# Performance work log

Hardware: AMD Instinct MI355X
Metric: run time of the kernel (lower is better)

Reference implementation:

```python
import jax, jax.numpy as jnp
import numpy as np

N = 50000          # nodes
E = 800000         # edges (avg degree 16)
DIN = 128          # d_input
H = 8              # heads per layer
D = 16             # per-head hidden dim
HID = H * D        # 128
ALPHA = 0.2        # LeakyReLU negative slope in GAT attention
BN_EPS = 1e-5


def _xavier(key, shape):
    fan_in, fan_out = shape[0], shape[-1]
    lim = np.sqrt(6.0 / (fan_in + fan_out)).astype(np.float32)
    return jax.random.uniform(key, shape, jnp.float32, -lim, lim)


def setup_inputs() -> dict:
    key = jax.random.key(0)
    ks = jax.random.split(key, 8)
    x = jax.random.normal(ks[0], (N, DIN), jnp.float32)
    edge_idx = jax.random.randint(ks[1], (2, E), 0, N)
    W1 = _xavier(ks[2], (DIN, HID))
    a1 = _xavier(ks[3], (H, 2 * D))
    W2 = _xavier(ks[4], (HID, HID))
    a2 = _xavier(ks[5], (H, 2 * D))
    W3 = _xavier(ks[6], (HID, HID))
    a3 = _xavier(ks[7], (H, 2 * D))
    ones = jnp.ones((HID,), jnp.float32)
    zeros = jnp.zeros((HID,), jnp.float32)
    return {"x": x, "edge_idx": edge_idx,
            "W1": W1, "a1": a1, "W2": W2, "a2": a2, "W3": W3, "a3": a3,
            "g1": ones, "b1": zeros, "g2": ones, "b2": zeros, "g3": ones, "b3": zeros}


def _leaky(x):
    return jnp.where(x >= 0, x, ALPHA * x)


def _gat_layer(x, src, dst, W, a):
    # x: [N, Fin]; W: [Fin, H*D]; a: [H, 2D]
    h = (x @ W).reshape(-1, H, D)                       # [N, H, D]
    e_src = jnp.einsum('nhd,hd->nh', h, a[:, :D])       # a^T part for source node
    e_dst = jnp.einsum('nhd,hd->nh', h, a[:, D:])       # a^T part for destination node
    e = _leaky(e_src[src] + e_dst[dst])                 # [E, H]
    m = jax.ops.segment_max(e, dst, num_segments=N)     # per-dst stable softmax max
    m = jnp.where(jnp.isfinite(m), m, 0.0)              # empty segments -> 0
    w = jnp.exp(e - m[dst])                             # [E, H]
    den = jax.ops.segment_sum(w, dst, num_segments=N)   # [N, H]
    agg = jax.ops.segment_sum(h[src] * w[:, :, None], dst, num_segments=N)  # [N, H, D]
    out = agg / (den[:, :, None] + 1e-16)
    return out.reshape(-1, HID)                         # concat heads


def _bn(x, g, b):
    # BatchNorm1d training-mode math over the node axis
    mu = x.mean(axis=0)
    var = x.var(axis=0)
    return g * (x - mu) * jax.lax.rsqrt(var + BN_EPS) + b


def reference(x, edge_idx, W1, a1, W2, a2, W3, a3, g1, b1, g2, b2, g3, b3):
    src, dst = edge_idx[0], edge_idx[1]
    h1 = jax.nn.elu(_bn(_gat_layer(x, src, dst, W1, a1), g1, b1))
    h2 = jax.nn.elu(_bn(_gat_layer(h1, src, dst, W2, a2), g2, b2))
    h3_in = h1 + h2  # skip connection
    return _bn(_gat_layer(h3_in, src, dst, W3, a3), g3, b3)
```

## Files before the change

### kernel.cpp

```cpp
#include <hip/hip_runtime.h>
#include <hip/hip_bf16.h>
#include <hip/hip_fp16.h>
#include <cstddef>

#define NNODES 50000
#define NEDGES 800000
#define HID 128
#define NHEAD 8
#define AGG_NB (NNODES / 4)
#define NSLICE 64
#define SLAYER (NSLICE * 512)

#define NBUCK 196
#define BCH 2048
#define BIN_NB ((NEDGES + BCH - 1) / BCH)

typedef __attribute__((ext_vector_type(4))) float floatx4;
typedef _Float16 __attribute__((ext_vector_type(8))) half8;
typedef _Float16 __attribute__((ext_vector_type(2))) half2v;

static inline size_t align_up(size_t x, size_t a) { return (x + a - 1) & ~(a - 1); }

__device__ inline float fexp2(float x) {
#if __has_builtin(__builtin_amdgcn_exp2f)
    return __builtin_amdgcn_exp2f(x);
#else
    return __expf(x * 0.69314718055994531f);
#endif
}

__device__ inline unsigned short f2h(float f) {
    return __builtin_bit_cast(unsigned short, (_Float16)f);
}

__global__ __launch_bounds__(256) void init_kernel(const float* __restrict__ W1,
                                                   const float* __restrict__ W2,
                                                   const float* __restrict__ W3,
                                                   unsigned short* __restrict__ Wt,
                                                   int* __restrict__ zeroA, int nA,
                                                   float* __restrict__ zeroB, int nB) {
    int b = blockIdx.x;
    int t = threadIdx.x;
    if (b < 192) {
        int layer = b >> 6;
        const float* W = (layer == 0) ? W1 : ((layer == 1) ? W2 : W3);
        int idx = (b & 63) * 256 + t;
        int n = idx & 127;
        int k = idx >> 7;
        Wt[layer * 16384 + n * 128 + k] = f2h(W[idx]);
    } else {
        int nb = gridDim.x - 192;
        int bb = b - 192;
        for (int i = bb * 256 + t; i < nA; i += nb * 256) zeroA[i] = 0;
        for (int i = bb * 256 + t; i < nB; i += nb * 256) zeroB[i] = 0.f;
    }
}

__global__ __launch_bounds__(256) void bin_count_kernel(const int* __restrict__ edge,
                                                        int* __restrict__ bucketCnt) {
    __shared__ int h[NBUCK];
    int t = threadIdx.x;
    if (t < NBUCK) h[t] = 0;
    __syncthreads();
    for (int i = blockIdx.x * 256 + t; i < NEDGES; i += gridDim.x * 256)
        atomicAdd(&h[edge[NEDGES + i] >> 8], 1);
    __syncthreads();
    if (t < NBUCK && h[t]) atomicAdd(&bucketCnt[t], h[t]);
}

__global__ __launch_bounds__(256) void bin_scatter_kernel(const int* __restrict__ edge,
                                                          const int* __restrict__ bucketCnt,
                                                          int* __restrict__ bucketCursor,
                                                          unsigned int* __restrict__ binned) {
    __shared__ int sA[256];
    __shared__ int hcnt[NBUCK];
    __shared__ int hbase[NBUCK];
    __shared__ int gbase[NBUCK];
    __shared__ unsigned int sEnt[BCH];
    __shared__ unsigned char sBk[BCH];
    int t = threadIdx.x;
    int e0 = blockIdx.x * BCH;
    int nv = NEDGES - e0;
    if (nv > BCH) nv = BCH;

    int gcnt = (t < NBUCK) ? bucketCnt[t] : 0;
    sA[t] = gcnt;
    __syncthreads();
    for (int off = 1; off < 256; off <<= 1) {
        int x = (t >= off) ? sA[t - off] : 0;
        __syncthreads();
        sA[t] += x;
        __syncthreads();
    }
    int gExBase = sA[t] - gcnt;
    if (t < NBUCK) hcnt[t] = 0;
    __syncthreads();

    int myB[8];
    int myR[8];
    unsigned int myP[8];
    #pragma unroll
    for (int j = 0; j < 8; ++j) {
        int idx = j * 256 + t;
        myB[j] = -1;
        if (idx < nv) {
            int s = edge[e0 + idx];
            int d = edge[NEDGES + e0 + idx];
            int bk = d >> 8;
            myB[j] = bk;
            myP[j] = (unsigned)s | ((unsigned)(d & 255) << 16);
            myR[j] = atomicAdd(&hcnt[bk], 1);
        }
    }
    __syncthreads();
    int hc = (t < NBUCK) ? hcnt[t] : 0;
    sA[t] = hc;
    __syncthreads();
    for (int off = 1; off < 256; off <<= 1) {
        int x = (t >= off) ? sA[t - off] : 0;
        __syncthreads();
        sA[t] += x;
        __syncthreads();
    }
    if (t < NBUCK) {
        hbase[t] = sA[t] - hc;
        gbase[t] = gExBase + atomicAdd(&bucketCursor[t], hc);
    }
    __syncthreads();
    #pragma unroll
    for (int j = 0; j < 8; ++j) {
        if (myB[j] >= 0) {
            int p = hbase[myB[j]] + myR[j];
            sEnt[p] = myP[j];
            sBk[p] = (unsigned char)myB[j];
        }
    }
    __syncthreads();
    #pragma unroll
    for (int j = 0; j < 8; ++j) {
        int i = j * 256 + t;
        if (i < nv) {
            int bk = sBk[i];
            binned[gbase[bk] + (i - hbase[bk])] = sEnt[i];
        }
    }
}

__global__ __launch_bounds__(256) void fine_csr_kernel(const int* __restrict__ bucketCnt,
                                                       const unsigned int* __restrict__ binned,
                                                       int* __restrict__ offs,
                                                       int* __restrict__ csr) {
    __shared__ int sA[256];
    __shared__ int sB[256];
    int t = threadIdx.x;
    int b = blockIdx.x;
    int v = (t < NBUCK) ? bucketCnt[t] : 0;
    sA[t] = v;
    __syncthreads();
    for (int off = 1; off < 256; off <<= 1) {
        int x = (t >= off) ? sA[t - off] : 0;
        __syncthreads();
        sA[t] += x;
        __syncthreads();
    }
    int cntb = bucketCnt[b];
    int base = sA[b] - cntb;
    sB[t] = 0;
    __syncthreads();
    for (int i = t; i < cntb; i += 256)
        atomicAdd(&sB[(binned[base + i] >> 16) & 255], 1);
    __syncthreads();
    int nc = sB[t];
    sA[t] = nc;
    __syncthreads();
    for (int off = 1; off < 256; off <<= 1) {
        int x = (t >= off) ? sA[t - off] : 0;
        __syncthreads();
        sA[t] += x;
        __syncthreads();
    }
    int nodeBase = base + sA[t] - nc;
    int gid = b * 256 + t;
    if (gid < NNODES) offs[gid] = nodeBase;
    if (b == NBUCK - 1 && t == 0) offs[NNODES] = NEDGES;
    sB[t] = nodeBase;
    __syncthreads();
    for (int i = t; i < cntb; i += 256) {
        unsigned e = binned[base + i];
        int pos = atomicAdd(&sB[(e >> 16) & 255], 1);
        csr[pos] = (int)(e & 0xFFFFu);
    }
}

#define GROWS 64
#define ASTRIDE 136
#define LOG2E 1.4426950408889634f
__global__ __launch_bounds__(256) void gemm_kernel(const float* __restrict__ Xin,
                                                   const float* __restrict__ skip,
                                                   const float* __restrict__ statsPart,
                                                   const float* __restrict__ g,
                                                   const float* __restrict__ b,
                                                   const unsigned short* __restrict__ Wt,
                                                   const float* __restrict__ a,
                                                   float* __restrict__ Hw,
                                                   unsigned short* __restrict__ Hb,
                                                   float* __restrict__ esrc,
                                                   float* __restrict__ edst,
                                                   int mode) {
    __shared__ unsigned short As[GROWS * ASTRIDE];
    __shared__ unsigned short Bs[128 * ASTRIDE];
    __shared__ float ssm[256];
    int tid = threadIdx.x;
    int rowBase = blockIdx.x * GROWS;

    for (int i = tid; i < 128 * 16; i += 256) {
        int n = i >> 4, seg = i & 15;
        *(uint4*)(&Bs[n * ASTRIDE + seg * 8]) = *(const uint4*)(Wt + n * 128 + seg * 8);
    }

    if (mode >= 1) {
        if (tid < 128) {
            float s = 0.f, s2 = 0.f;
            #pragma unroll 8
            for (int k = 0; k < NSLICE; ++k) {
                s  += statsPart[k * 512 + tid];
                s2 += statsPart[k * 512 + 128 + tid];
            }
            float mu = s / (float)NNODES;
            float var = s2 / (float)NNODES - mu * mu;
            float rstd = rsqrtf(var + 1e-5f);
            float scale = g[tid] * rstd;
            ssm[tid] = scale;
            ssm[128 + tid] = b[tid] - mu * scale;
        }
        __syncthreads();
    }

    {
        int r = tid >> 2;
        int cs = (tid & 3) * 32;
        int gr = rowBase + r;
        float4 vv[8];
        if (gr < NNODES) {
            #pragma unroll
            for (int j = 0; j < 8; ++j)
                vv[j] = *(const float4*)(Xin + (size_t)gr * HID + cs + j * 4);
            if (mode >= 1) {
                #pragma unroll
                for (int j = 0; j < 8; ++j) {
                    int ch = cs + j * 4;
                    float4 sc = *(const float4*)(ssm + ch);
                    float4 sh = *(const float4*)(ssm + 128 + ch);
                    float4 v = vv[j];
                    v.x = sc.x * v.x + sh.x;
                    v.y = sc.y * v.y + sh.y;
                    v.z = sc.z * v.z + sh.z;
                    v.w = sc.w * v.w + sh.w;
                    v.x = (v.x > 0.f) ? v.x : expm1f(v.x);
                    v.y = (v.y > 0.f) ? v.y : expm1f(v.y);
                    v.z = (v.z > 0.f) ? v.z : expm1f(v.z);
                    v.w = (v.w > 0.f) ? v.w : expm1f(v.w);
                    if (mode == 2) {
                        float4 s = *(const float4*)(skip + (size_t)gr * HID + ch);
                        v.x += s.x; v.y += s.y; v.z += s.z; v.w += s.w;
                    }
                    vv[j] = v;
                }
                if (mode == 1) {
                    #pragma unroll
                    for (int j = 0; j < 8; ++j)
                        *(float4*)(Hw + (size_t)gr * HID + cs + j * 4) = vv[j];
                }
            }
        } else {
            #pragma unroll
            for (int j = 0; j < 8; ++j) vv[j] = make_float4(0.f, 0.f, 0.f, 0.f);
        }
        unsigned int pk[16];
        #pragma unroll
        for (int j = 0; j < 8; ++j) {
            pk[2 * j]     = __builtin_bit_cast(unsigned int,
                                __builtin_amdgcn_cvt_pkrtz(vv[j].x, vv[j].y));
            pk[2 * j + 1] = __builtin_bit_cast(unsigned int,
                                __builtin_amdgcn_cvt_pkrtz(vv[j].z, vv[j].w));
        }
        #pragma unroll
        for (int q = 0; q < 4; ++q)
            *(uint4*)(&As[r * ASTRIDE + cs + q * 8]) =
                make_uint4(pk[4 * q], pk[4 * q + 1], pk[4 * q + 2], pk[4 * q + 3]);
    }
    __syncthreads();

    int wv = tid >> 6;
    int lane = tid & 63;
    int l15 = lane & 15;
    int quad = lane >> 4;
    const unsigned short* Arow = &As[(wv * 16 + l15) * ASTRIDE + quad * 8];
    half8 af[4];
    #pragma unroll
    for (int c = 0; c < 4; ++c) af[c] = *(const half8*)(Arow + c * 32);

    floatx4 acc[8];
    #pragma unroll
    for (int h = 0; h < 8; ++h) {
        acc[h] = (floatx4){0.f, 0.f, 0.f, 0.f};
        const unsigned short* Brow = &Bs[(h * 16 + l15) * ASTRIDE + quad * 8];
        #pragma unroll
        for (int c = 0; c < 4; ++c) {
            half8 bfr = *(const half8*)(Brow + c * 32);
            acc[h] = __builtin_amdgcn_mfma_f32_16x16x32_f16(af[c], bfr, acc[h], 0, 0, 0);
        }
    }
    __syncthreads();

    #pragma unroll
    for (int h = 0; h < 8; ++h) {
        #pragma unroll
        for (int reg = 0; reg < 4; ++reg)
            As[(wv * 16 + quad * 4 + reg) * ASTRIDE + h * 16 + l15] = f2h(acc[h][reg]);
    }
    __syncthreads();

    {
        int r = tid >> 2;
        int hp = tid & 3;
        int gr = rowBase + r;
        const unsigned short* row = &As[r * ASTRIDE + hp * 32];
        uint4 u[4];
        #pragma unroll
        for (int q = 0; q < 4; ++q) u[q] = *(const uint4*)(row + q * 8);
        if (gr < NNODES) {
            uint4* dst = (uint4*)(Hb + (size_t)gr * HID + hp * 32);
            #pragma unroll
            for (int q = 0; q < 4; ++q) dst[q] = u[q];
            float f[32];
            #pragma unroll
            for (int q = 0; q < 4; ++q) {
                unsigned int* pu = (unsigned int*)&u[q];
                #pragma unroll
                for (int j = 0; j < 4; ++j) {
                    half2v hv = __builtin_bit_cast(half2v, pu[j]);
                    f[q * 8 + 2 * j]     = (float)hv[0];
                    f[q * 8 + 2 * j + 1] = (float)hv[1];
                }
            }
            int h0 = hp * 2, h1 = hp * 2 + 1;
            float es0 = 0.f, ev0 = 0.f, es1 = 0.f, ev1 = 0.f;
            #pragma unroll
            for (int j = 0; j < 16; ++j) {
                es0 += f[j] * a[h0 * 32 + j];
                ev0 += f[j] * a[h0 * 32 + 16 + j];
                es1 += f[16 + j] * a[h1 * 32 + j];
                ev1 += f[16 + j] * a[h1 * 32 + 16 + j];
            }
            esrc[gr * NHEAD + h0] = es0 * LOG2E;
            esrc[gr * NHEAD + h1] = es1 * LOG2E;
            edst[gr * NHEAD + h0] = ev0 * LOG2E;
            edst[gr * NHEAD + h1] = ev1 * LOG2E;
        }
    }
}

__global__ __launch_bounds__(256) void aggregate_kernel(const int* __restrict__ offs,
                                                        const int* __restrict__ csr,
                                                        const float* __restrict__ esrc,
                                                        const float* __restrict__ edst,
                                                        const unsigned int* __restrict__ Hb,
                                                        float* __restrict__ out,
                                                        float* __restrict__ statsPart) {
    int tid = threadIdx.x;
    int wv = tid >> 6;
    int n = blockIdx.x * 4 + wv;
    int lane = tid & 63;
    int head = lane >> 3;
    int beg = offs[n], end = offs[n + 1];
    float ed = edst[n * NHEAD + head];
    float acc0 = 0.f, acc1 = 0.f, den = 0.f;
    for (int i = beg; i < end; i += 16) {
        int ss[16];
        #pragma unroll
        for (int j = 0; j < 16; ++j) {
            int k = min(i + j, end - 1);
            ss[j] = csr[k];
        }
        float ee[16];
        unsigned int hh[16];
        #pragma unroll
        for (int j = 0; j < 16; ++j)
            ee[j] = esrc[(unsigned)ss[j] * 8u + (unsigned)head];
        #pragma unroll
        for (int j = 0; j < 16; ++j)
            hh[j] = Hb[(unsigned)ss[j] * 64u + (unsigned)lane];
        #pragma unroll
        for (int j = 0; j < 16; ++j) {
            float e = ee[j] + ed;
            e = fmaxf(e, 0.2f * e);
            float w = fexp2(e);
            w = (i + j < end) ? w : 0.f;
            den += w;
            half2v h2 = __builtin_bit_cast(half2v, hh[j]);
            acc0 += w * (float)h2[0];
            acc1 += w * (float)h2[1];
        }
    }
    float inv = 1.f / (den + 1e-16f);
    float o0 = acc0 * inv;
    float o1 = acc1 * inv;
    *(float2*)(out + (size_t)n * HID + lane * 2) = make_float2(o0, o1);

    __shared__ float sm[4][128];
    *(float2*)(&sm[wv][lane * 2]) = make_float2(o0, o1);
    __syncthreads();
    if (tid < 128) {
        float a0 = sm[0][tid], a1 = sm[1][tid], a2 = sm[2][tid], a3 = sm[3][tid];
        float s = a0 + a1 + a2 + a3;
        float s2 = a0 * a0 + a1 * a1 + a2 * a2 + a3 * a3;
        float* slice = statsPart + (blockIdx.x & (NSLICE - 1)) * 512;
        atomicAdd(&slice[tid], s);
        atomicAdd(&slice[128 + tid], s2);
    }
}

__global__ __launch_bounds__(256) void final_apply_kernel(const float* __restrict__ X,
                                                          const float* __restrict__ statsPart,
                                                          const float* __restrict__ g,
                                                          const float* __restrict__ b,
                                                          float* __restrict__ out) {
    __shared__ float ssm[256];
    int tid = threadIdx.x;
    if (tid < 128) {
        float s = 0.f, s2 = 0.f;
        #pragma unroll 8
        for (int k = 0; k < NSLICE; ++k) {
            s  += statsPart[k * 512 + tid];
            s2 += statsPart[k * 512 + 128 + tid];
        }
        float mu = s / (float)NNODES;
        float var = s2 / (float)NNODES - mu * mu;
        float rstd = rsqrtf(var + 1e-5f);
        float scale = g[tid] * rstd;
        ssm[tid] = scale;
        ssm[128 + tid] = b[tid] - mu * scale;
    }
    __syncthreads();
    int total4 = NNODES * HID / 4;
    for (int i = blockIdx.x * 256 + tid; i < total4; i += gridDim.x * 256) {
        float4 v = ((const float4*)X)[i];
        int c4 = (i & 31) * 4;
        float4 sc = *(const float4*)(ssm + c4);
        float4 sh = *(const float4*)(ssm + 128 + c4);
        v.x = sc.x * v.x + sh.x;
        v.y = sc.y * v.y + sh.y;
        v.z = sc.z * v.z + sh.z;
        v.w = sc.w * v.w + sh.w;
        ((float4*)out)[i] = v;
    }
}

extern "C" void kernel_launch(void* const* d_in, const int* in_sizes, int n_in,
                              void* d_out, int out_size, void* d_ws, size_t ws_size,
                              hipStream_t stream) {
    const float* x   = (const float*)d_in[0];
    const int* edge  = (const int*)d_in[1];
    const float* W1  = (const float*)d_in[2];
    const float* a1  = (const float*)d_in[3];
    const float* W2  = (const float*)d_in[4];
    const float* a2  = (const float*)d_in[5];
    const float* W3  = (const float*)d_in[6];
    const float* a3  = (const float*)d_in[7];
    const float* g1  = (const float*)d_in[8];
    const float* b1  = (const float*)d_in[9];
    const float* g2  = (const float*)d_in[10];
    const float* b2  = (const float*)d_in[11];
    const float* g3  = (const float*)d_in[12];
    const float* b3  = (const float*)d_in[13];
    float* outp      = (float*)d_out;

    char* p = (char*)d_ws;
    size_t cur = 0;
    auto carve = [&](size_t bytes) {
        void* r = p + cur;
        cur = align_up(cur + bytes, 256);
        return r;
    };
    int*   offs   = (int*)carve((NNODES + 1) * sizeof(int));
    int*   csr    = (int*)carve(NEDGES * sizeof(int));
    unsigned short* wt = (unsigned short*)carve(3 * 16384 * sizeof(unsigned short));
    unsigned short* hb = (unsigned short*)carve((size_t)NNODES * HID * sizeof(unsigned short));
    float* agg    = (float*)carve((size_t)NNODES * HID * sizeof(float));
    float* h1     = (float*)carve((size_t)NNODES * HID * sizeof(float));
    float* esrc   = (float*)carve((size_t)NNODES * NHEAD * sizeof(float));
    float* edst   = (float*)carve((size_t)NNODES * NHEAD * sizeof(float));
    float* stats  = (float*)carve(3 * SLAYER * sizeof(float));
    int*   bcnt   = (int*)carve(2 * NBUCK * sizeof(int));
    int*   bcur   = bcnt + NBUCK;
    float* stats1 = stats;
    float* stats2 = stats + SLAYER;
    float* stats3 = stats + 2 * SLAYER;
    unsigned int* binned = (unsigned int*)h1;

    const int GB = (NNODES + GROWS - 1) / GROWS;

    init_kernel<<<256, 256, 0, stream>>>(W1, W2, W3, wt,
                                         bcnt, 2 * NBUCK,
                                         stats, 3 * SLAYER);
    bin_count_kernel<<<256, 256, 0, stream>>>(edge, bcnt);
    bin_scatter_kernel<<<BIN_NB, 256, 0, stream>>>(edge, bcnt, bcur, binned);
    fine_csr_kernel<<<NBUCK, 256, 0, stream>>>(bcnt, binned, offs, csr);

    gemm_kernel<<<GB, 256, 0, stream>>>(x, nullptr, nullptr, nullptr, nullptr,
                                        wt, a1, nullptr, hb, esrc, edst, 0);
    aggregate_kernel<<<AGG_NB, 256, 0, stream>>>(offs, csr, esrc, edst,
                                                 (const unsigned int*)hb, agg, stats1);

    gemm_kernel<<<GB, 256, 0, stream>>>(agg, nullptr, stats1, g1, b1,
                                        wt + 16384, a2, h1, hb, esrc, edst, 1);
    aggregate_kernel<<<AGG_NB, 256, 0, stream>>>(offs, csr, esrc, edst,
                                                 (const unsigned int*)hb, agg, stats2);

    gemm_kernel<<<GB, 256, 0, stream>>>(agg, h1, stats2, g2, b2,
                                        wt + 32768, a3, nullptr, hb, esrc, edst, 2);
    aggregate_kernel<<<AGG_NB, 256, 0, stream>>>(offs, csr, esrc, edst,
                                                 (const unsigned int*)hb, agg, stats3);

    final_apply_kernel<<<768, 256, 0, stream>>>(agg, stats3, g3, b3, outp);
}
```

Before: 377.5 us.

## Process four nodes per wavefront in GAT aggregation with 16-byte gathers

The aggregation kernel now assigns 16 lanes per destination node, so each wavefront handles four nodes. Each lane loads 8 fp16 features as a uint4 and keeps 8 accumulators, and edges are processed 4 at a time instead of 16. The aim is wider gather loads, fewer wasted padded iterations for low-degree nodes, and a quarter as many blocks and stats atomics. In exchange, each lane holds more registers, and nodes with different degrees share a wavefront, which can cause divergence.

```diff
diff --git a/kernel.cpp b/kernel.cpp
--- a/kernel.cpp
+++ b/kernel.cpp
@@ -7,7 +7,7 @@
 #define NEDGES 800000
 #define HID 128
 #define NHEAD 8
-#define AGG_NB (NNODES / 4)
+#define AGG_NB (NNODES / 16)
 #define NSLICE 64
 #define SLAYER (NSLICE * 512)
 
@@ -370,51 +370,71 @@
                                                         float* __restrict__ statsPart) {
     int tid = threadIdx.x;
     int wv = tid >> 6;
-    int n = blockIdx.x * 4 + wv;
     int lane = tid & 63;
-    int head = lane >> 3;
+    int grp = lane >> 4;
+    int sub = lane & 15;
+    int head = sub >> 1;
+    int n = blockIdx.x * 16 + wv * 4 + grp;
     int beg = offs[n], end = offs[n + 1];
     float ed = edst[n * NHEAD + head];
-    float acc0 = 0.f, acc1 = 0.f, den = 0.f;
-    for (int i = beg; i < end; i += 16) {
-        int ss[16];
-        #pragma unroll
-        for (int j = 0; j < 16; ++j) {
-            int k = min(i + j, end - 1);
-            ss[j] = csr[k];
-        }
-        float ee[16];
-        unsigned int hh[16];
-        #pragma unroll
-        for (int j = 0; j < 16; ++j)
+    float acc[8];
+    #pragma unroll
+    for (int q = 0; q < 8; ++q) acc[q] = 0.f;
+    float den = 0.f;
+    for (int i = beg; i < end; i += 4) {
+        int ss[4];
+        #pragma unroll
+        for (int j = 0; j < 4; ++j)
+            ss[j] = csr[min(i + j, end - 1)];
+        float ee[4];
+        uint4 hh[4];
+        #pragma unroll
+        for (int j = 0; j < 4; ++j)
             ee[j] = esrc[(unsigned)ss[j] * 8u + (unsigned)head];
         #pragma unroll
-        for (int j = 0; j < 16; ++j)
-            hh[j] = Hb[(unsigned)ss[j] * 64u + (unsigned)lane];
-        #pragma unroll
-        for (int j = 0; j < 16; ++j) {
+        for (int j = 0; j < 4; ++j)
+            hh[j] = *(const uint4*)(Hb + (unsigned)ss[j] * 64u + (unsigned)sub * 4u);
+        #pragma unroll
+        for (int j = 0; j < 4; ++j) {
             float e = ee[j] + ed;
             e = fmaxf(e, 0.2f * e);
             float w = fexp2(e);
             w = (i + j < end) ? w : 0.f;
             den += w;
-            half2v h2 = __builtin_bit_cast(half2v, hh[j]);
-            acc0 += w * (float)h2[0];
-            acc1 += w * (float)h2[1];
+            half2v h0 = __builtin_bit_cast(half2v, hh[j].x);
+            half2v h1 = __builtin_bit_cast(half2v, hh[j].y);
+            half2v h2 = __builtin_bit_cast(half2v, hh[j].z);
+            half2v h3 = __builtin_bit_cast(half2v, hh[j].w);
+            acc[0] += w * (float)h0[0];
+            acc[1] += w * (float)h0[1];
+            acc[2] += w * (float)h1[0];
+            acc[3] += w * (float)h1[1];
+            acc[4] += w * (float)h2[0];
+            acc[5] += w * (float)h2[1];
+            acc[6] += w * (float)h3[0];
+            acc[7] += w * (float)h3[1];
         }
     }
     float inv = 1.f / (den + 1e-16f);
-    float o0 = acc0 * inv;
-    float o1 = acc1 * inv;
-    *(float2*)(out + (size_t)n * HID + lane * 2) = make_float2(o0, o1);
-
-    __shared__ float sm[4][128];
-    *(float2*)(&sm[wv][lane * 2]) = make_float2(o0, o1);
+    float4 o0 = make_float4(acc[0] * inv, acc[1] * inv, acc[2] * inv, acc[3] * inv);
+    float4 o1 = make_float4(acc[4] * inv, acc[5] * inv, acc[6] * inv, acc[7] * inv);
+    float* orow = out + (size_t)n * HID + sub * 8;
+    *(float4*)orow = o0;
+    *(float4*)(orow + 4) = o1;
+
+    __shared__ float sm[16 * 136];
+    float* srow = &sm[(wv * 4 + grp) * 136 + sub * 8];
+    *(float4*)srow = o0;
+    *(float4*)(srow + 4) = o1;
     __syncthreads();
     if (tid < 128) {
-        float a0 = sm[0][tid], a1 = sm[1][tid], a2 = sm[2][tid], a3 = sm[3][tid];
-        float s = a0 + a1 + a2 + a3;
-        float s2 = a0 * a0 + a1 * a1 + a2 * a2 + a3 * a3;
+        float s = 0.f, s2 = 0.f;
+        #pragma unroll
+        for (int r = 0; r < 16; ++r) {
+            float v = sm[r * 136 + tid];
+            s += v;
+            s2 += v * v;
+        }
         float* slice = statsPart + (blockIdx.x & (NSLICE - 1)) * 512;
         atomicAdd(&slice[tid], s);
         atomicAdd(&slice[128 + tid], s2);
```

New measurement: 362.0 us. 4.1% less time.
